# Optimization experiments

Hardware: AMD Instinct MI355X
Metric: run time of the kernel (lower is better)

## Reference

```python
import jax, jax.numpy as jnp
import numpy as np

N_NODES = 100000
N_EDGES = 3200000


def gcn_conv(x, W, b, row, col, n):
    # PyG GCNConv: add self-loops, symmetric normalization D^-1/2 (A+I) D^-1/2 (X W) + b
    xw = x @ W  # [N, out]
    loops = jnp.arange(n)
    row2 = jnp.concatenate([row, loops])
    col2 = jnp.concatenate([col, loops])
    deg = jax.ops.segment_sum(jnp.ones_like(col2, dtype=xw.dtype), col2, num_segments=n)
    dinv = jnp.where(deg > 0, jax.lax.rsqrt(deg), 0.0)
    norm = dinv[row2] * dinv[col2]  # [E+N]
    msg = xw[row2] * norm[:, None]  # gather + scale
    out = jax.ops.segment_sum(msg, col2, num_segments=n)  # scatter-add to targets
    return out + b


def setup_inputs() -> dict:
    key = jax.random.key(0)
    ks = jax.random.split(key, 9)
    x = jax.random.normal(ks[0], (N_NODES, 2), dtype=jnp.float32)
    edge_index = jax.random.randint(ks[1], (2, N_EDGES), 0, N_NODES, dtype=jnp.int64)
    edge_attr = jax.random.normal(ks[2], (N_EDGES, 1), dtype=jnp.float32)
    # params (glorot-ish scale)
    W1 = jax.random.normal(ks[3], (2, 16), dtype=jnp.float32) * (1.0 / np.sqrt(2))
    b1 = jnp.zeros((16,), dtype=jnp.float32)
    We = jax.random.normal(ks[4], (33, 4), dtype=jnp.float32) * (1.0 / np.sqrt(33))
    be = jnp.zeros((4,), dtype=jnp.float32)
    W2 = jax.random.normal(ks[5], (16, 2), dtype=jnp.float32) * (1.0 / np.sqrt(16))
    b2 = jnp.zeros((2,), dtype=jnp.float32)
    return {"x": x, "edge_index": edge_index, "edge_attr": edge_attr,
            "W1": W1, "b1": b1, "We": We, "be": be, "W2": W2, "b2": b2}


def reference(x, edge_index, edge_attr, W1, b1, We, be, W2, b2):
    row, col = edge_index[0], edge_index[1]
    n = x.shape[0]
    h = gcn_conv(x, W1, b1, row, col, n)  # [N, 16]
    # edge update: gather src/dst features, concat with edge_attr, Linear+ReLU
    e_in = jnp.concatenate([h[row], edge_attr, h[col]], axis=1)  # [E, 33]
    e_out = jax.nn.relu(e_in @ We + be)  # [E, 4]
    out_x = gcn_conv(h, W2, b2, row, col, n)  # [N, 2]
    return jax.nn.log_softmax(out_x, axis=1), jax.nn.log_softmax(e_out, axis=1)
```

## Files before the change

### kernel.cpp

```cpp
#include <hip/hip_runtime.h>


#define BLK 256
#define CH 8192
#define BSH 7
#define BSZ 128
#define NBMAX 1024
#define S1 262144.0f
#define S2 65536.0f
#define BIAS 8388608

__global__ void k_hist(const int* __restrict__ col, int* __restrict__ gcount,
                       int E, int NB) {
    __shared__ int hist[NBMAX];
    int t = threadIdx.x;
    for (int b = t; b < NB; b += BLK) hist[b] = 0;
    __syncthreads();
    int e0 = blockIdx.x * CH;
    int cnt = min(CH, E - e0);
    for (int k = t; k < cnt; k += BLK)
        atomicAdd(&hist[col[e0 + k] >> BSH], 1);
    __syncthreads();
    for (int b = t; b < NB; b += BLK) {
        int h = hist[b];
        if (h) atomicAdd(&gcount[b], h);
    }
}

__global__ void k_scan(const int* __restrict__ gcount, int* __restrict__ gbase,
                       int* __restrict__ gcursor, int NB) {
    __shared__ int sa[NBMAX], sb[NBMAX];
    int t = threadIdx.x;
    for (int i = t; i < NBMAX; i += BLK) sa[i] = (i < NB) ? gcount[i] : 0;
    __syncthreads();
    int *src = sa, *dst = sb;
    for (int off = 1; off < NBMAX; off <<= 1) {
        for (int i = t; i < NBMAX; i += BLK)
            dst[i] = src[i] + ((i >= off) ? src[i - off] : 0);
        __syncthreads();
        int* tmp = src; src = dst; dst = tmp;
    }
    for (int i = t; i < NB; i += BLK) {
        int ex = src[i] - gcount[i];
        gbase[i] = ex;
        gcursor[i] = ex;
    }
    if (t == 0) gbase[NB] = src[NB - 1];
}

__global__ void k_part(const int* __restrict__ row, const int* __restrict__ col,
                       int* __restrict__ gcursor, unsigned* __restrict__ part,
                       int E, int NB) {
    __shared__ int sa[NBMAX], sb[NBMAX];
    __shared__ int hist[NBMAX], lstart[NBMAX], lcur[NBMAX], gb[NBMAX];
    __shared__ unsigned sbuf[CH];
    __shared__ unsigned short bid[CH];
    int t = threadIdx.x;
    int e0 = blockIdx.x * CH;
    int cnt = min(CH, E - e0);
    for (int b = t; b < NB; b += BLK) hist[b] = 0;
    __syncthreads();
    for (int k = t; k < cnt; k += BLK)
        atomicAdd(&hist[col[e0 + k] >> BSH], 1);
    __syncthreads();
    for (int i = t; i < NBMAX; i += BLK) sa[i] = (i < NB) ? hist[i] : 0;
    __syncthreads();
    int *src = sa, *dst = sb;
    for (int off = 1; off < NBMAX; off <<= 1) {
        for (int i = t; i < NBMAX; i += BLK)
            dst[i] = src[i] + ((i >= off) ? src[i - off] : 0);
        __syncthreads();
        int* tmp = src; src = dst; dst = tmp;
    }
    for (int i = t; i < NB; i += BLK) {
        int h = hist[i];
        int ex = src[i] - h;
        lstart[i] = ex;
        lcur[i] = ex;
        gb[i] = h ? atomicAdd(&gcursor[i], h) : 0;
    }
    __syncthreads();
    for (int k = t; k < cnt; k += BLK) {
        int e = e0 + k;
        int c = col[e], r = row[e];
        int b = c >> BSH;
        int off = atomicAdd(&lcur[b], 1);
        sbuf[off] = ((unsigned)r << BSH) | (unsigned)(c & (BSZ - 1));
        bid[off] = (unsigned short)b;
    }
    __syncthreads();
    for (int j = t; j < cnt; j += BLK) {
        int b = bid[j];
        part[gb[b] + (j - lstart[b])] = sbuf[j];
    }
}

__global__ void k_nodeA(const unsigned* __restrict__ part, const int* __restrict__ gbase,
                        const float2* __restrict__ x2, float* __restrict__ dinv,
                        int* __restrict__ degi, int2* __restrict__ pi, int N) {
    __shared__ int cnt[BSZ];
    int t = threadIdx.x;
    if (t < BSZ) cnt[t] = 0;
    __syncthreads();
    int b = blockIdx.x;
    int j0 = gbase[b], j1 = gbase[b + 1];
    for (int j = j0 + t; j < j1; j += BLK)
        atomicAdd(&cnt[part[j] & (BSZ - 1)], 1);
    __syncthreads();
    if (t < BSZ) {
        int node = (b << BSH) + t;
        if (node < N) {
            int dg = cnt[t];
            degi[node] = dg;
            float d = rsqrtf((float)(dg + 1));
            dinv[node] = d;
            float2 xv = x2[node];
            pi[node] = make_int2(__float2int_rn(xv.x * d * S1),
                                 __float2int_rn(xv.y * d * S1));
        }
    }
}

__global__ void k_nodeB(const unsigned* __restrict__ part, const int* __restrict__ gbase,
                        const float* __restrict__ dinv, const int* __restrict__ degi,
                        const int2* __restrict__ pi,
                        const float* __restrict__ W1, const float* __restrict__ b1,
                        const float* __restrict__ W2, const float* __restrict__ We,
                        const float* __restrict__ be,
                        float4* __restrict__ U, float4* __restrict__ V,
                        int2* __restrict__ qi, int N) {
    __shared__ unsigned long long acc[BSZ];
    __shared__ float sW1[32], sb1[16], sW2[32], sWr[64], sWc[64], sbe[4];
    int t = threadIdx.x;
    if (t < BSZ) acc[t] = 0ull;
    if (t < 32) sW1[t] = W1[t];
    else if (t < 64) sW2[t - 32] = W2[t - 32];
    else if (t < 80) sb1[t - 64] = b1[t - 64];
    else if (t < 144) sWr[t - 80] = We[t - 80];
    else if (t < 208) sWc[t - 144] = We[68 + (t - 144)];
    else if (t < 212) sbe[t - 208] = be[t - 208];
    __syncthreads();
    int b = blockIdx.x;
    int j0 = gbase[b], j1 = gbase[b + 1];
    for (int j = j0 + t; j < j1; j += BLK) {
        unsigned w = part[j];
        int2 pv = pi[w >> BSH];
        int l = (int)(w & (BSZ - 1));
        unsigned long long val =
            ((unsigned long long)(unsigned)pv.x << 32) | (unsigned)(pv.y + BIAS);
        atomicAdd(&acc[l], val);
    }
    __syncthreads();
    if (t < BSZ) {
        int node = (b << BSH) + t;
        if (node < N) {
            unsigned long long a = acc[t];
            int sx = (int)(unsigned)(a >> 32);
            long long sy = (long long)(unsigned)(a & 0xffffffffull)
                         - (long long)degi[node] * BIAS;
            int2 ps = pi[node];
            float d = dinv[node];
            float ax = (float)(ps.x + (long long)sx) * (1.0f / S1);
            float ay = (float)(ps.y + sy) * (1.0f / S1);
            float s0 = d * ax, s1 = d * ay;
            float u0 = sbe[0], u1 = sbe[1], u2 = sbe[2], u3 = sbe[3];
            float v0 = 0.f, v1 = 0.f, v2 = 0.f, v3 = 0.f;
            float w0 = 0.f, w1 = 0.f;
            #pragma unroll
            for (int jj = 0; jj < 16; jj++) {
                float hj = fmaf(s0, sW1[jj], fmaf(s1, sW1[16 + jj], sb1[jj]));
                u0 = fmaf(hj, sWr[4 * jj + 0], u0);
                u1 = fmaf(hj, sWr[4 * jj + 1], u1);
                u2 = fmaf(hj, sWr[4 * jj + 2], u2);
                u3 = fmaf(hj, sWr[4 * jj + 3], u3);
                v0 = fmaf(hj, sWc[4 * jj + 0], v0);
                v1 = fmaf(hj, sWc[4 * jj + 1], v1);
                v2 = fmaf(hj, sWc[4 * jj + 2], v2);
                v3 = fmaf(hj, sWc[4 * jj + 3], v3);
                w0 = fmaf(hj, sW2[2 * jj], w0);
                w1 = fmaf(hj, sW2[2 * jj + 1], w1);
            }
            U[node] = make_float4(u0, u1, u2, u3);
            V[node] = make_float4(v0, v1, v2, v3);
            float qx = w0 * d, qy = w1 * d;
            qi[node] = make_int2(__float2int_rn(qx * S2), __float2int_rn(qy * S2));
        }
    }
}

__global__ void k_edge(const int* __restrict__ row, const int* __restrict__ col,
                       const float* __restrict__ ea, const float4* __restrict__ U,
                       const float4* __restrict__ V, const float* __restrict__ We,
                       float4* __restrict__ eout, int E) {
    __shared__ float sW16[4];
    int t = threadIdx.x;
    if (t < 4) sW16[t] = We[64 + t];
    __syncthreads();
    int e = blockIdx.x * BLK + t;
    if (e < E) {
        float4 u = U[row[e]];
        float4 v = V[col[e]];
        float av = ea[e];
        float a0 = u.x + fmaf(av, sW16[0], v.x);
        float a1 = u.y + fmaf(av, sW16[1], v.y);
        float a2 = u.z + fmaf(av, sW16[2], v.z);
        float a3 = u.w + fmaf(av, sW16[3], v.w);
        a0 = fmaxf(a0, 0.f); a1 = fmaxf(a1, 0.f);
        a2 = fmaxf(a2, 0.f); a3 = fmaxf(a3, 0.f);
        float m = fmaxf(fmaxf(a0, a1), fmaxf(a2, a3));
        float s = expf(a0 - m) + expf(a1 - m) + expf(a2 - m) + expf(a3 - m);
        float l = m + logf(s);
        eout[e] = make_float4(a0 - l, a1 - l, a2 - l, a3 - l);
    }
}

__global__ void k_nodeC(const unsigned* __restrict__ part, const int* __restrict__ gbase,
                        const float* __restrict__ dinv, const int* __restrict__ degi,
                        const int2* __restrict__ qi,
                        const float* __restrict__ b2, float2* __restrict__ outn, int N) {
    __shared__ unsigned long long acc[BSZ];
    int t = threadIdx.x;
    if (t < BSZ) acc[t] = 0ull;
    __syncthreads();
    int b = blockIdx.x;
    int j0 = gbase[b], j1 = gbase[b + 1];
    for (int j = j0 + t; j < j1; j += BLK) {
        unsigned w = part[j];
        int2 qv = qi[w >> BSH];
        int l = (int)(w & (BSZ - 1));
        unsigned long long val =
            ((unsigned long long)(unsigned)qv.x << 32) | (unsigned)(qv.y + BIAS);
        atomicAdd(&acc[l], val);
    }
    __syncthreads();
    if (t < BSZ) {
        int node = (b << BSH) + t;
        if (node < N) {
            unsigned long long a = acc[t];
            int sx = (int)(unsigned)(a >> 32);
            long long sy = (long long)(unsigned)(a & 0xffffffffull)
                         - (long long)degi[node] * BIAS;
            int2 qs = qi[node];
            float d = dinv[node];
            float bx = (float)(qs.x + (long long)sx) * (1.0f / S2);
            float by = (float)(qs.y + sy) * (1.0f / S2);
            float o0 = fmaf(d, bx, b2[0]);
            float o1 = fmaf(d, by, b2[1]);
            float m = fmaxf(o0, o1);
            float l2 = m + logf(expf(o0 - m) + expf(o1 - m));
            outn[node] = make_float2(o0 - l2, o1 - l2);
        }
    }
}

extern "C" void kernel_launch(void* const* d_in, const int* in_sizes, int n_in,
                              void* d_out, int out_size, void* d_ws, size_t ws_size,
                              hipStream_t stream) {
    const float* x  = (const float*)d_in[0];
    const int*   ei = (const int*)d_in[1];
    const float* ea = (const float*)d_in[2];
    const float* W1 = (const float*)d_in[3];
    const float* b1 = (const float*)d_in[4];
    const float* We = (const float*)d_in[5];
    const float* be = (const float*)d_in[6];
    const float* W2 = (const float*)d_in[7];
    const float* b2 = (const float*)d_in[8];

    const int N = in_sizes[0] / 2;
    const int E = in_sizes[2];
    const int* row = ei;
    const int* col = ei + E;
    const int NB  = (N + BSZ - 1) >> BSH;
    const int NCH = (E + CH - 1) / CH;

    float2* out_nodes = (float2*)d_out;
    float4* out_edges = (float4*)((float*)d_out + 2 * (size_t)N);

    char* ws = (char*)d_ws;
    int*      gcount  = (int*)     (ws + 0);
    int*      gbase   = (int*)     (ws + 4096);
    int*      gcursor = (int*)     (ws + 12288);
    float*    dinv    = (float*)   (ws + 16384);
    int*      degi    = (int*)     (ws + 416384);
    int2*     pi      = (int2*)    (ws + 816384);
    int2*     qi      = (int2*)    (ws + 1616384);
    float4*   U       = (float4*)  (ws + 2416384);
    float4*   V       = (float4*)  (ws + 4016384);
    unsigned* part    = (unsigned*)(ws + 5616384);

    hipMemsetAsync(gcount, 0, NBMAX * sizeof(int), stream);
    k_hist <<<NCH, BLK, 0, stream>>>(col, gcount, E, NB);
    k_scan <<<1,   BLK, 0, stream>>>(gcount, gbase, gcursor, NB);
    k_part <<<NCH, BLK, 0, stream>>>(row, col, gcursor, part, E, NB);
    k_nodeA<<<NB,  BLK, 0, stream>>>(part, gbase, (const float2*)x, dinv, degi, pi, N);
    k_nodeB<<<NB,  BLK, 0, stream>>>(part, gbase, dinv, degi, pi, W1, b1, W2, We, be, U, V, qi, N);
    k_edge <<<(E + BLK - 1) / BLK, BLK, 0, stream>>>(row, col, ea, U, V, We, out_edges, E);
    k_nodeC<<<NB,  BLK, 0, stream>>>(part, gbase, dinv, degi, qi, b2, out_nodes, N);
}
```

Baseline: 249.6 us.

## Halve partition chunk size, use wave-shuffle scan, cache col in registers

Halves the edges per partition block, which doubles the number of blocks and cuts shared memory per block. The 10-step Hillis-Steele shared-memory scan over 1024 bins is replaced by a per-thread 4-bin sum plus a wavefront shuffle scan. Column indices are kept in registers between the histogram and scatter passes so they are not read from global memory twice. The cost is more blocks doing global cursor atomics, and the CH change also alters chunking in k_hist.

```diff
diff --git a/kernel.cpp b/kernel.cpp
--- a/kernel.cpp
+++ b/kernel.cpp
@@ -2,7 +2,8 @@
 
 
 #define BLK 256
-#define CH 8192
+#define CH 4096
+#define EPT (CH / BLK)
 #define BSH 7
 #define BSZ 128
 #define NBMAX 1024
@@ -51,47 +52,72 @@
 __global__ void k_part(const int* __restrict__ row, const int* __restrict__ col,
                        int* __restrict__ gcursor, unsigned* __restrict__ part,
                        int E, int NB) {
-    __shared__ int sa[NBMAX], sb[NBMAX];
-    __shared__ int hist[NBMAX], lstart[NBMAX], lcur[NBMAX], gb[NBMAX];
+    __shared__ __align__(16) int hist[NBMAX];
+    __shared__ __align__(16) int lstart[NBMAX];
+    __shared__ __align__(16) int lcur[NBMAX];
+    __shared__ int gb[NBMAX];
     __shared__ unsigned sbuf[CH];
     __shared__ unsigned short bid[CH];
+    __shared__ int wsum[BLK / 64];
     int t = threadIdx.x;
     int e0 = blockIdx.x * CH;
     int cnt = min(CH, E - e0);
-    for (int b = t; b < NB; b += BLK) hist[b] = 0;
-    __syncthreads();
-    for (int k = t; k < cnt; k += BLK)
-        atomicAdd(&hist[col[e0 + k] >> BSH], 1);
-    __syncthreads();
-    for (int i = t; i < NBMAX; i += BLK) sa[i] = (i < NB) ? hist[i] : 0;
-    __syncthreads();
-    int *src = sa, *dst = sb;
-    for (int off = 1; off < NBMAX; off <<= 1) {
-        for (int i = t; i < NBMAX; i += BLK)
-            dst[i] = src[i] + ((i >= off) ? src[i - off] : 0);
-        __syncthreads();
-        int* tmp = src; src = dst; dst = tmp;
-    }
-    for (int i = t; i < NB; i += BLK) {
-        int h = hist[i];
-        int ex = src[i] - h;
-        lstart[i] = ex;
-        lcur[i] = ex;
-        gb[i] = h ? atomicAdd(&gcursor[i], h) : 0;
-    }
-    __syncthreads();
-    for (int k = t; k < cnt; k += BLK) {
-        int e = e0 + k;
-        int c = col[e], r = row[e];
-        int b = c >> BSH;
-        int off = atomicAdd(&lcur[b], 1);
-        sbuf[off] = ((unsigned)r << BSH) | (unsigned)(c & (BSZ - 1));
-        bid[off] = (unsigned short)b;
-    }
-    __syncthreads();
-    for (int j = t; j < cnt; j += BLK) {
-        int b = bid[j];
-        part[gb[b] + (j - lstart[b])] = sbuf[j];
+    for (int i = t; i < NBMAX; i += BLK) hist[i] = 0;
+    __syncthreads();
+    int cv[EPT];
+    #pragma unroll
+    for (int i = 0; i < EPT; i++) {
+        int k = t + i * BLK;
+        if (k < cnt) {
+            int c = col[e0 + k];
+            cv[i] = c;
+            atomicAdd(&hist[c >> BSH], 1);
+        }
+    }
+    __syncthreads();
+    int i0 = 4 * t;
+    int4 hv = reinterpret_cast<const int4*>(hist)[t];
+    int h0 = hv.x, h1 = hv.y, h2 = hv.z, h3 = hv.w;
+    int s1 = h0 + h1, s2 = s1 + h2, s3 = s2 + h3;
+    int lane = t & 63, wid = t >> 6;
+    int v = s3;
+    #pragma unroll
+    for (int off = 1; off < 64; off <<= 1) {
+        int u = __shfl_up(v, off);
+        if (lane >= off) v += u;
+    }
+    if (lane == 63) wsum[wid] = v;
+    __syncthreads();
+    int base = v - s3;
+    for (int w = 0; w < wid; w++) base += wsum[w];
+    int ex0 = base, ex1 = base + h0, ex2 = base + s1, ex3 = base + s2;
+    reinterpret_cast<int4*>(lstart)[t] = make_int4(ex0, ex1, ex2, ex3);
+    reinterpret_cast<int4*>(lcur)[t]   = make_int4(ex0, ex1, ex2, ex3);
+    gb[i0]     = h0 ? atomicAdd(&gcursor[i0],     h0) : 0;
+    gb[i0 + 1] = h1 ? atomicAdd(&gcursor[i0 + 1], h1) : 0;
+    gb[i0 + 2] = h2 ? atomicAdd(&gcursor[i0 + 2], h2) : 0;
+    gb[i0 + 3] = h3 ? atomicAdd(&gcursor[i0 + 3], h3) : 0;
+    __syncthreads();
+    #pragma unroll
+    for (int i = 0; i < EPT; i++) {
+        int k = t + i * BLK;
+        if (k < cnt) {
+            int c = cv[i];
+            int r = row[e0 + k];
+            int b = c >> BSH;
+            int off = atomicAdd(&lcur[b], 1);
+            sbuf[off] = ((unsigned)r << BSH) | (unsigned)(c & (BSZ - 1));
+            bid[off] = (unsigned short)b;
+        }
+    }
+    __syncthreads();
+    #pragma unroll
+    for (int i = 0; i < EPT; i++) {
+        int j = t + i * BLK;
+        if (j < cnt) {
+            int b = bid[j];
+            part[gb[b] + (j - lstart[b])] = sbuf[j];
+        }
     }
 }
 
```

Measured after the change: 290.7 us. 16.5% more time.
